# Kernel tuning notes

Measured on AMD Instinct MI355X. Metric: run time of the kernel, lower is better.

The kernel has to match this reference:

```python
import jax, jax.numpy as jnp
import numpy as np

H, D, RPE_DIM, LAYERS = 8, 64, 64, 3
B, N = 8, 4096
EPS = 1e-8


def _srms(x):
    # SimpleRMSNorm: x / (||x||_2 / sqrt(d) + eps) == x / (rms(x) + eps)
    rms = jnp.sqrt(jnp.mean(x * x, axis=-1, keepdims=True))
    return x / (rms + EPS)


def _rpe(pos, w_in, b_in, w_layers, b_layers, w_out, b_out):
    # pos: [nf, 1] -> [nf, H*2*D]
    x = pos @ w_in + b_in
    for i in range(LAYERS):  # fixed small layer count
        x = jax.nn.relu(_srms(x)) @ w_layers[i] + b_layers[i]
    return jax.nn.relu(_srms(x)) @ w_out + b_out


def setup_inputs() -> dict:
    key = jax.random.key(0)
    ks = jax.random.split(key, 4)
    s = 0.02
    return {
        "x": jax.random.normal(ks[0], (B, H, N, D), jnp.float32),
        "w_in": jax.random.normal(ks[1], (1, RPE_DIM), jnp.float32) * s,
        "b_in": jnp.zeros((RPE_DIM,), jnp.float32),
        "w_layers": jax.random.normal(ks[2], (LAYERS, RPE_DIM, RPE_DIM), jnp.float32) * s,
        "b_layers": jnp.zeros((LAYERS, RPE_DIM), jnp.float32),
        "w_out": jax.random.normal(ks[3], (RPE_DIM, H * 2 * D), jnp.float32) * s,
        "b_out": jnp.zeros((H * 2 * D,), jnp.float32),
    }


def reference(x, w_in, b_in, w_layers, b_layers, w_out, b_out):
    # x: [b, h, n, d]; non-causal TnoFD with act_type='none' (identity act_fun)
    n = x.shape[-2]
    fft_size = 2 * n
    nf = fft_size // 2 + 1  # n + 1 frequencies
    pos = jnp.linspace(0.0, np.pi, nf, dtype=x.dtype).reshape(nf, 1)
    res = _rpe(pos, w_in, b_in, w_layers, b_layers, w_out, b_out)  # [nf, H*2D]
    # rearrange 'n (h d) -> h n d'
    res = res.reshape(nf, H, 2 * D).transpose(1, 0, 2)  # [H, nf, 2D]
    real, imag = res[..., :D], res[..., D:]
    imag = imag.at[:, 0, :].set(0.0).at[:, -1, :].set(0.0)
    a = real + 1j * imag  # [H, nf, D] complex filter
    y = jnp.fft.rfft(x, n=fft_size, axis=-2)  # [b, H, nf, D]
    out = jnp.fft.irfft(a * y, n=fft_size, axis=-2)[:, :, :n, :]
    return out.astype(x.dtype)
```

## Files before the change

kernel.cpp:

```cpp
#include <hip/hip_runtime.h>
#include <math.h>


#define PI_F 3.14159265358979323846f
#define TWO_PI_F 6.283185307179586f

__device__ __forceinline__ int r8(int k) {
    return ((k & 7) << 3) | (k >> 3);
}

__global__ __launch_bounds__(512) void gen_tw_kernel(float2* __restrict__ tw4096,
                                                     float2* __restrict__ tw8192,
                                                     float2* __restrict__ e64)
{
    int idx = blockIdx.x * 512 + threadIdx.x;
    if (idx < 4096) {
        float s, c; __sincosf(TWO_PI_F * (float)idx * (1.0f / 4096.0f), &s, &c);
        tw4096[idx] = make_float2(c, s);
    } else if (idx < 8192) {
        int j = idx - 4096;
        float s, c; __sincosf(TWO_PI_F * (float)j * (1.0f / 8192.0f), &s, &c);
        tw8192[j] = make_float2(c, s);
    } else if (idx < 8256) {
        int j = idx - 8192;
        float s, c; __sincosf(TWO_PI_F * (float)j * (1.0f / 64.0f), &s, &c);
        e64[j] = make_float2(c, s);
    }
}

__device__ __forceinline__ void fft8_regs(float2* v, float sgn) {
    float t0r = v[0].x + v[4].x, t0i = v[0].y + v[4].y;
    float t1r = v[0].x - v[4].x, t1i = v[0].y - v[4].y;
    float t2r = v[2].x + v[6].x, t2i = v[2].y + v[6].y;
    float t3r = v[2].x - v[6].x, t3i = v[2].y - v[6].y;
    float e0r = t0r + t2r, e0i = t0i + t2i;
    float e2r = t0r - t2r, e2i = t0i - t2i;
    float e1r = t1r - sgn * t3i, e1i = t1i + sgn * t3r;
    float e3r = t1r + sgn * t3i, e3i = t1i - sgn * t3r;
    float u0r = v[1].x + v[5].x, u0i = v[1].y + v[5].y;
    float u1r = v[1].x - v[5].x, u1i = v[1].y - v[5].y;
    float u2r = v[3].x + v[7].x, u2i = v[3].y + v[7].y;
    float u3r = v[3].x - v[7].x, u3i = v[3].y - v[7].y;
    float o0r = u0r + u2r, o0i = u0i + u2i;
    float o2r = u0r - u2r, o2i = u0i - u2i;
    float o1r = u1r - sgn * u3i, o1i = u1i + sgn * u3r;
    float o3r = u1r + sgn * u3i, o3i = u1i - sgn * u3r;
    const float C = 0.70710678118654752f;
    float w1r = C * (o1r - sgn * o1i), w1i = C * (o1i + sgn * o1r);
    float w2r = -sgn * o2i,            w2i = sgn * o2r;
    float w3r = -C * (o3r + sgn * o3i), w3i = C * (sgn * o3r - o3i);
    v[0] = make_float2(e0r + o0r, e0i + o0i);
    v[4] = make_float2(e0r - o0r, e0i - o0i);
    v[1] = make_float2(e1r + w1r, e1i + w1i);
    v[5] = make_float2(e1r - w1r, e1i - w1i);
    v[2] = make_float2(e2r + w2r, e2i + w2i);
    v[6] = make_float2(e2r - w2r, e2i - w2i);
    v[3] = make_float2(e3r + w3r, e3i + w3i);
    v[7] = make_float2(e3r - w3r, e3i - w3i);
}

__device__ __forceinline__ void fft64_dif(float2* zz, int col, int j0, float sgn,
                                          bool act, const float2* e64s) {
    if (act) {
        #pragma unroll
        for (int jj = 0; jj < 2; ++jj) {
            const int j = j0 + jj * 4;
            float2 v[8];
            #pragma unroll
            for (int r = 0; r < 8; ++r) v[r] = zz[(8 * r + j) * 64 + col];
            fft8_regs(v, sgn);
            #pragma unroll
            for (int r = 1; r < 8; ++r) {
                float2 t = e64s[j * r];
                float c = t.x, s = sgn * t.y;
                float vr = v[r].x, vi = v[r].y;
                v[r] = make_float2(vr * c - vi * s, vr * s + vi * c);
            }
            #pragma unroll
            for (int r = 0; r < 8; ++r) zz[(8 * r + j) * 64 + col] = v[r];
        }
    }
    __syncthreads();
    if (act) {
        #pragma unroll
        for (int jj = 0; jj < 2; ++jj) {
            const int j = j0 + jj * 4;
            float2 v[8];
            #pragma unroll
            for (int r = 0; r < 8; ++r) v[r] = zz[(8 * j + r) * 64 + col];
            fft8_regs(v, sgn);
            #pragma unroll
            for (int r = 0; r < 8; ++r) zz[(8 * j + r) * 64 + col] = v[r];
        }
    }
    __syncthreads();
}

__device__ __forceinline__ void fft64_dit(float2* zz, int col, int j0, float sgn,
                                          bool act, const float2* e64s) {
    if (act) {
        #pragma unroll
        for (int jj = 0; jj < 2; ++jj) {
            const int j = j0 + jj * 4;
            float2 v[8];
            #pragma unroll
            for (int r = 0; r < 8; ++r) v[r] = zz[(8 * j + r) * 64 + col];
            fft8_regs(v, sgn);
            #pragma unroll
            for (int r = 1; r < 8; ++r) {
                float2 t = e64s[j * r];
                float c = t.x, s = sgn * t.y;
                float vr = v[r].x, vi = v[r].y;
                v[r] = make_float2(vr * c - vi * s, vr * s + vi * c);
            }
            #pragma unroll
            for (int r = 0; r < 8; ++r) zz[(8 * j + r) * 64 + col] = v[r];
        }
    }
    __syncthreads();
    if (act) {
        #pragma unroll
        for (int jj = 0; jj < 2; ++jj) {
            const int j = j0 + jj * 4;
            float2 v[8];
            #pragma unroll
            for (int r = 0; r < 8; ++r) v[r] = zz[(8 * r + j) * 64 + col];
            fft8_regs(v, sgn);
            #pragma unroll
            for (int r = 0; r < 8; ++r) zz[(8 * r + j) * 64 + col] = v[r];
        }
    }
    __syncthreads();
}

__global__ __launch_bounds__(256) void mlp_hidden_kernel(
    const float* __restrict__ w_in, const float* __restrict__ b_in,
    const float* __restrict__ w_layers, const float* __restrict__ b_layers,
    float* __restrict__ rbuf)
{
    const int lane = threadIdx.x & 63;
    const int k = blockIdx.x * 4 + (threadIdx.x >> 6);
    if (k > 4096) return;
    const float pos = PI_F * (float)k * (1.0f / 4096.0f);
    float xv = fmaf(pos, w_in[lane], b_in[lane]);
    for (int l = 0; l < 3; ++l) {
        float ss = xv * xv;
        #pragma unroll
        for (int o = 1; o < 64; o <<= 1) ss += __shfl_xor(ss, o, 64);
        float r = xv / (sqrtf(ss * (1.0f / 64.0f)) + 1e-8f);
        r = fmaxf(r, 0.0f);
        const float* W = w_layers + l * 4096;
        float a0 = 0.f, a1 = 0.f, a2 = 0.f, a3 = 0.f;
        for (int i = 0; i < 64; i += 4) {
            a0 = fmaf(__shfl(r, i, 64),     W[(i) * 64 + lane],     a0);
            a1 = fmaf(__shfl(r, i + 1, 64), W[(i + 1) * 64 + lane], a1);
            a2 = fmaf(__shfl(r, i + 2, 64), W[(i + 2) * 64 + lane], a2);
            a3 = fmaf(__shfl(r, i + 3, 64), W[(i + 3) * 64 + lane], a3);
        }
        xv = ((a0 + a1) + (a2 + a3)) + b_layers[l * 64 + lane];
    }
    float ss = xv * xv;
    #pragma unroll
    for (int o = 1; o < 64; o <<= 1) ss += __shfl_xor(ss, o, 64);
    float r = xv / (sqrtf(ss * (1.0f / 64.0f)) + 1e-8f);
    r = fmaxf(r, 0.0f);
    rbuf[(size_t)k * 64 + lane] = r;
}

__global__ __launch_bounds__(256) void mlp_out_kernel(
    const float* __restrict__ rbuf, const float* __restrict__ w_out,
    const float* __restrict__ b_out, float* __restrict__ res)
{
    __shared__ float rl[16 * 64];
    const int tid = threadIdx.x;
    const int nt = blockIdx.x, kt = blockIdx.y;
    for (int it = 0; it < 4; ++it) {
        int idx = it * 256 + tid;
        int row = idx >> 6, i = idx & 63;
        int k = kt * 16 + row;
        rl[idx] = (k <= 4096) ? rbuf[(size_t)k * 64 + i] : 0.0f;
    }
    __syncthreads();
    const int n = nt * 256 + tid;
    float acc[16];
    #pragma unroll
    for (int j = 0; j < 16; ++j) acc[j] = 0.0f;
    for (int i = 0; i < 64; ++i) {
        float wv = w_out[(size_t)i * 1024 + n];
        #pragma unroll
        for (int j = 0; j < 16; ++j)
            acc[j] = fmaf(rl[j * 64 + i], wv, acc[j]);
    }
    float bv = b_out[n];
    for (int j = 0; j < 16; ++j) {
        int k = kt * 16 + j;
        if (k <= 4096) res[(size_t)k * 1024 + n] = acc[j] + bv;
    }
}

__global__ __launch_bounds__(256) void fwd1_kernel(const float* __restrict__ x,
                                                   float2* __restrict__ Y,
                                                   const float2* __restrict__ tw4096,
                                                   const float2* __restrict__ e64g,
                                                   int slab_base)
{
    __shared__ float2 zz[4096];
    __shared__ float2 e64s[64];
    __shared__ float2 twA[64];
    const int tid = threadIdx.x;
    const int m0 = blockIdx.x, lslab = blockIdx.y;
    if (tid < 64) e64s[tid] = e64g[tid];
    else if (tid < 128) twA[tid - 64] = tw4096[m0 * (tid - 64)];
    const float* xs = x + (size_t)(slab_base + lslab) * 262144;
    for (int it = 0; it < 16; ++it) {
        int slot = it * 256 + tid;
        int m1 = slot >> 6, d = slot & 63;
        if (m1 < 32) {
            float vr = xs[(size_t)(128 * m1 + 2 * m0) * 64 + d];
            float vi = xs[(size_t)(128 * m1 + 2 * m0 + 1) * 64 + d];
            zz[slot] = make_float2(vr, vi);
        } else {
            zz[slot] = make_float2(0.0f, 0.0f);
        }
    }
    __syncthreads();
    const int col = tid & 63, j0 = tid >> 6;
    fft64_dif(zz, col, j0, -1.0f, true, e64s);
    float2* Ys = Y + (size_t)lslab * 262144 + (size_t)m0 * 64;
    for (int og = 0; og < 16; ++og) {
        int k1 = og * 4 + j0;
        float2 v = zz[r8(k1) * 64 + col];
        float2 t = twA[k1];
        float c = t.x, s = -t.y;
        Ys[(size_t)k1 * 4096 + col] = make_float2(v.x * c - v.y * s,
                                                  v.x * s + v.y * c);
    }
}

__global__ __launch_bounds__(256) void midspec_kernel(float2* __restrict__ Y,
                                                      const float* __restrict__ res,
                                                      const float2* __restrict__ tw4096,
                                                      const float2* __restrict__ tw8192,
                                                      const float2* __restrict__ e64g,
                                                      int slab_base)
{
    __shared__ float2 zz[4096];
    __shared__ float2 e64s[64];
    __shared__ float2 twS[64];
    __shared__ float2 twB[128];
    const int tid = threadIdx.x;
    const int bx = blockIdx.x;
    const int k1p = bx >> 1, dh = bx & 1;
    const int lslab = blockIdx.y;
    const int h = (slab_base + lslab) & 7;
    const bool pairwg = (k1p >= 1 && k1p <= 31);
    const int k1a = k1p;
    const int k1b = pairwg ? (64 - k1p) : k1p;
    const int NC = pairwg ? 64 : 32;

    if (tid < 64) e64s[tid] = e64g[tid];
    else if (tid < 128) twS[tid - 64] = tw8192[(tid - 64) * 64 + k1a];
    else {
        int i = tid - 128;
        int kk1 = (i < 64) ? k1a : k1b;
        twB[i] = tw4096[(i & 63) * kk1];
    }

    const float4* Pa4 = (const float4*)(Y + (size_t)lslab * 262144 + (size_t)k1a * 4096);
    for (int it = 0; it < 4; ++it) {
        int idx4 = it * 256 + tid;
        int m0 = idx4 >> 4, f = idx4 & 15;
        float4 v = Pa4[m0 * 32 + 16 * dh + f];
        *(float4*)&zz[m0 * 64 + 2 * f] = v;
    }
    if (pairwg) {
        const float4* Pb4 = (const float4*)(Y + (size_t)lslab * 262144 + (size_t)k1b * 4096);
        for (int it = 0; it < 4; ++it) {
            int idx4 = it * 256 + tid;
            int m0 = idx4 >> 4, f = idx4 & 15;
            float4 v = Pb4[m0 * 32 + 16 * dh + f];
            *(float4*)&zz[m0 * 64 + 32 + 2 * f] = v;
        }
    }
    __syncthreads();
    const int col = tid & 63, j0 = tid >> 6;
    fft64_dif(zz, col, j0, -1.0f, col < NC, e64s);

    const int nit = pairwg ? 8 : 4;
    for (int it = 0; it < nit; ++it) {
        int item = it * 256 + tid;
        int k0 = item >> 5, dl = item & 31;
        int c = h * 128 + 32 * dh + dl;
        if (k1p == 0 && k0 == 0) {
            float2 C0 = zz[dl];
            float X0 = C0.x + C0.y, XN = C0.x - C0.y;
            float a0 = res[c], aN = res[(size_t)4096 * 1024 + c];
            float S0 = a0 * X0, SN = aN * XN;
            zz[dl] = make_float2(0.5f * (S0 + SN), 0.5f * (S0 - SN));
            int p2 = 4 * 64 + dl;
            float2 Cq = zz[p2];
            float ar = res[(size_t)2048 * 1024 + c], ai = res[(size_t)2048 * 1024 + c + 64];
            float Sr = ar * Cq.x + ai * Cq.y;
            float Si = ai * Cq.x - ar * Cq.y;
            zz[p2] = make_float2(Sr, -Si);
        } else {
            int k0p, coff;
            if (pairwg)          { k0p = 63 - k0;        coff = 32; }
            else if (k1p == 0)   { k0p = (64 - k0) & 63; coff = 0;  }
            else  { k0p = 63 - k0;        coff = 0;  }
            int sa = r8(k0)  * 64 + dl;
            int sb = r8(k0p) * 64 + coff + dl;
            int k  = k0 * 64 + k1a;
            int km = 4096 - k;
            float2 Ck = zz[sa], Cm = zz[sb];
            float Er = 0.5f * (Ck.x + Cm.x), Ei = 0.5f * (Ck.y - Cm.y);
            float Dr = 0.5f * (Ck.x - Cm.x), Di = 0.5f * (Ck.y + Cm.y);
            float Or = Di, Oi = -Dr;
            float2 tk = twS[k0];
            float cw = tk.x, sw = -tk.y;
            float Tr = Or * cw - Oi * sw, Ti = Or * sw + Oi * cw;
            float Xkr = Er + Tr, Xki = Ei + Ti;
            float Xmr = Er - Tr, Xmi = Ti - Ei;
            float akr = res[(size_t)k * 1024 + c],  aki = res[(size_t)k * 1024 + c + 64];
            float amr = res[(size_t)km * 1024 + c], ami = res[(size_t)km * 1024 + c + 64];
            float Skr = akr * Xkr - aki * Xki, Ski = akr * Xki + aki * Xkr;
            float Smr = amr * Xmr - ami * Xmi, Smi = amr * Xmi + ami * Xmr;
            float Epr = 0.5f * (Skr + Smr), Epi = 0.5f * (Ski - Smi);
            float Ddr = 0.5f * (Skr - Smr), Ddi = 0.5f * (Ski + Smi);
            float Opr = Ddr * cw + Ddi * sw, Opi = Ddi * cw - Ddr * sw;
            zz[sa] = make_float2(Epr - Opi, Epi + Opr);
            zz[sb] = make_float2(Epr + Opi, Opr - Epi);
        }
    }
    __syncthreads();
    fft64_dit(zz, col, j0, +1.0f, col < NC, e64s);

    const int nit2 = pairwg ? 16 : 8;
    for (int it = 0; it < nit2; ++it) {
        int item = it * 256 + tid;
        int pl = item >> 11, rem = item & 2047;
        int m0 = rem >> 5, dl = rem & 31;
        int k1 = pl ? k1b : k1a;
        float2 v = zz[m0 * 64 + pl * 32 + dl];
        float2 t = twB[pl * 64 + m0];
        float c2 = t.x, s = t.y;
        Y[(size_t)lslab * 262144 + (size_t)k1 * 4096 + (size_t)m0 * 64 + 32 * dh + dl] =
            make_float2(v.x * c2 - v.y * s, v.x * s + v.y * c2);
    }
}

__global__ __launch_bounds__(256) void inv2_kernel(const float2* __restrict__ Y,
                                                   float* __restrict__ out,
                                                   const float2* __restrict__ e64g,
                                                   int slab_base)
{
    __shared__ float2 zz[4096];
    __shared__ float2 e64s[64];
    const int tid = threadIdx.x;
    const int m0 = blockIdx.x, lslab = blockIdx.y;
    if (tid < 64) e64s[tid] = e64g[tid];
    const float2* Ys = Y + (size_t)lslab * 262144 + (size_t)m0 * 64;
    const float4* Ys4 = (const float4*)Ys;
    for (int it = 0; it < 8; ++it) {
        int idx4 = it * 256 + tid;
        int k1 = idx4 >> 5, f = idx4 & 31;
        float4 v = Ys4[k1 * 2048 + f];
        *(float4*)&zz[k1 * 64 + 2 * f] = v;
    }
    __syncthreads();
    const int col = tid & 63, j0 = tid >> 6;
    fft64_dif(zz, col, j0, +1.0f, true, e64s);
    float* os = out + (size_t)(slab_base + lslab) * 262144;
    const float sc = 1.0f / 4096.0f;
    for (int it = 0; it < 8; ++it) {
        int slot = it * 256 + tid;
        int m1 = slot >> 6, d = slot & 63;
        float2 v = zz[r8(m1) * 64 + d];
        os[(size_t)(128 * m1 + 2 * m0) * 64 + d]     = v.x * sc;
        os[(size_t)(128 * m1 + 2 * m0 + 1) * 64 + d] = v.y * sc;
    }
}

#define PADF(i) ((i) + ((i) >> 5))

__device__ __forceinline__ unsigned dr4_12(unsigned k) {
    unsigned rb = __brev(k) >> 20;
    return ((rb & 0x555u) << 1) | ((rb >> 1) & 0x555u);
}

__global__ __launch_bounds__(64) void rpe_mlp_kernel(
    const float* __restrict__ w_in, const float* __restrict__ b_in,
    const float* __restrict__ w_layers, const float* __restrict__ b_layers,
    const float* __restrict__ w_out, const float* __restrict__ b_out,
    float* __restrict__ res)
{
    const int k = blockIdx.x;
    const int lane = threadIdx.x;
    const float pos = PI_F * (float)k * (1.0f / 4096.0f);
    float xv = fmaf(pos, w_in[lane], b_in[lane]);
    for (int l = 0; l < 3; ++l) {
        float ss = xv * xv;
        #pragma unroll
        for (int o = 1; o < 64; o <<= 1) ss += __shfl_xor(ss, o, 64);
        float rms = sqrtf(ss * (1.0f / 64.0f));
        float r = xv / (rms + 1e-8f);
        r = r > 0.0f ? r : 0.0f;
        const float* W = w_layers + l * 64 * 64;
        float acc = b_layers[l * 64 + lane];
        for (int i = 0; i < 64; ++i)
            acc = fmaf(__shfl(r, i, 64), W[i * 64 + lane], acc);
        xv = acc;
    }
    float ss = xv * xv;
    #pragma unroll
    for (int o = 1; o < 64; o <<= 1) ss += __shfl_xor(ss, o, 64);
    float rms = sqrtf(ss * (1.0f / 64.0f));
    float r = xv / (rms + 1e-8f);
    r = r > 0.0f ? r : 0.0f;
    float acc[16];
    #pragma unroll
    for (int u = 0; u < 16; ++u) acc[u] = b_out[u * 64 + lane];
    for (int i = 0; i < 64; ++i) {
        float rv = __shfl(r, i, 64);
        const float* Wrow = w_out + i * 1024;
        #pragma unroll
        for (int u = 0; u < 16; ++u)
            acc[u] = fmaf(rv, Wrow[u * 64 + lane], acc[u]);
    }
    float* dst = res + (size_t)k * 1024;
    #pragma unroll
    for (int u = 0; u < 16; ++u) dst[u * 64 + lane] = acc[u];
}

__global__ __launch_bounds__(256) void fftconv_kernel(
    const float* __restrict__ x, const float* __restrict__ res,
    float* __restrict__ out)
{
    __shared__ float re[PADF(4095) + 1];
    __shared__ float im[PADF(4095) + 1];
    const int tid = threadIdx.x;
    const int blk = blockIdx.x;
    const int d = (blk >> 3) & 63;
    const int slab = (blk & 7) | ((blk >> 9) << 3);
    const int h = slab & 7;
    const size_t base = (size_t)slab * 4096 * 64 + (size_t)d;
    const float* xc = x + base;
    float* oc = out + base;
    const int c = h * 128 + d;
    for (int m = tid; m < 2048; m += 256) {
        re[PADF(m)] = xc[(size_t)(2 * m) * 64];
        im[PADF(m)] = xc[(size_t)(2 * m + 1) * 64];
    }
    for (int m = 2048 + tid; m < 4096; m += 256) { re[PADF(m)] = 0.0f; im[PADF(m)] = 0.0f; }
    __syncthreads();
    for (int S = 1024; S >= 1; S >>= 2) {
        const float ab = -TWO_PI_F / (float)(4 * S);
        for (int j = tid; j < 1024; j += 256) {
            const int q = j & (S - 1);
            const int i0 = ((j & ~(S - 1)) << 2) | q;
            const int p0 = PADF(i0), p1 = PADF(i0 + S), p2 = PADF(i0 + 2 * S), p3 = PADF(i0 + 3 * S);
            float x0r = re[p0], x0i = im[p0], x1r = re[p1], x1i = im[p1];
            float x2r = re[p2], x2i = im[p2], x3r = re[p3], x3i = im[p3];
            float A0r = x0r + x2r, A0i = x0i + x2i, A1r = x0r - x2r, A1i = x0i - x2i;
            float A2r = x1r + x3r, A2i = x1i + x3i, A3r = x1r - x3r, A3i = x1i - x3i;
            float s1, c1; __sincosf(ab * (float)q, &s1, &c1);
            float c2 = c1 * c1 - s1 * s1, s2 = 2.0f * c1 * s1;
            float c3 = c2 * c1 - s2 * s1, s3 = s2 * c1 + c2 * s1;
            re[p0] = A0r + A2r; im[p0] = A0i + A2i;
            float t1r = A1r + A3i, t1i = A1i - A3r;
            re[p1] = t1r * c1 - t1i * s1; im[p1] = t1r * s1 + t1i * c1;
            float t2r = A0r - A2r, t2i = A0i - A2i;
            re[p2] = t2r * c2 - t2i * s2; im[p2] = t2r * s2 + t2i * c2;
            float t3r = A1r - A3i, t3i = A1i + A3r;
            re[p3] = t3r * c3 - t3i * s3; im[p3] = t3r * s3 + t3i * c3;
        }
        __syncthreads();
    }
    for (int k = tid; k <= 2048; k += 256) {
        if (k == 0) {
            float C0r = re[0], C0i = im[0];
            float X0 = C0r + C0i, XN = C0r - C0i;
            float a0 = res[c], aN = res[(size_t)4096 * 1024 + c];
            float S0 = a0 * X0, SN = aN * XN;
            re[0] = 0.5f * (S0 + SN); im[0] = 0.5f * (S0 - SN);
        } else if (k == 2048) {
            const int p = PADF(2);
            float Cr = re[p], Ci = im[p];
            float ar = res[(size_t)2048 * 1024 + c], ai = res[(size_t)2048 * 1024 + c + 64];
            float Sr = ar * Cr + ai * Ci, Si = ai * Cr - ar * Ci;
            re[p] = Sr; im[p] = -Si;
        } else {
            const int pk = PADF((int)dr4_12((unsigned)k));
            const int pm = PADF((int)dr4_12((unsigned)(4096 - k)));
            float Ckr = re[pk], Cki = im[pk];
            float Cmr = re[pm], Cmi = im[pm];
            float Er = 0.5f * (Ckr + Cmr), Ei = 0.5f * (Cki - Cmi);
            float Dr = 0.5f * (Ckr - Cmr), Di = 0.5f * (Cki + Cmi);
            float Or = Di, Oi = -Dr;
            float sw, cw; __sincosf(-TWO_PI_F * (float)k * (1.0f / 8192.0f), &sw, &cw);
            float Tr = Or * cw - Oi * sw, Ti = Or * sw + Oi * cw;
            float Xkr = Er + Tr, Xki = Ei + Ti;
            float Xmr = Er - Tr, Xmi = Ti - Ei;
            float akr = res[(size_t)k * 1024 + c], aki = res[(size_t)k * 1024 + c + 64];
            float amr = res[(size_t)(4096 - k) * 1024 + c], ami = res[(size_t)(4096 - k) * 1024 + c + 64];
            float Skr = akr * Xkr - aki * Xki, Ski = akr * Xki + aki * Xkr;
            float Smr = amr * Xmr - ami * Xmi, Smi = amr * Xmi + ami * Xmr;
            float Epr = 0.5f * (Skr + Smr), Epi = 0.5f * (Ski - Smi);
            float Ddr = 0.5f * (Skr - Smr), Ddi = 0.5f * (Ski + Smi);
            float Opr = Ddr * cw + Ddi * sw, Opi = Ddi * cw - Ddr * sw;
            re[pk] = Epr - Opi; im[pk] = Epi + Opr;
            re[pm] = Epr + Opi; im[pm] = Opr - Epi;
        }
    }
    __syncthreads();
    for (int S = 1; S <= 1024; S <<= 2) {
        const float ab = TWO_PI_F / (float)(4 * S);
        for (int j = tid; j < 1024; j += 256) {
            const int q = j & (S - 1);
            const int i0 = ((j & ~(S - 1)) << 2) | q;
            const int p0 = PADF(i0), p1 = PADF(i0 + S), p2 = PADF(i0 + 2 * S), p3 = PADF(i0 + 3 * S);
            float y0r = re[p0], y0i = im[p0], y1r = re[p1], y1i = im[p1];
            float y2r = re[p2], y2i = im[p2], y3r = re[p3], y3i = im[p3];
            float s1, c1; __sincosf(ab * (float)q, &s1, &c1);
            float c2 = c1 * c1 - s1 * s1, s2 = 2.0f * c1 * s1;
            float c3 = c2 * c1 - s2 * s1, s3 = s2 * c1 + c2 * s1;
            float x1r = y1r * c1 - y1i * s1, x1i = y1r * s1 + y1i * c1;
            float x2r = y2r * c2 - y2i * s2, x2i = y2r * s2 + y2i * c2;
            float x3r = y3r * c3 - y3i * s3, x3i = y3r * s3 + y3i * c3;
            float B0r = y0r + x2r, B0i = y0i + x2i, B1r = y0r - x2r, B1i = y0i - x2i;
            float B2r = x1r + x3r, B2i = x1i + x3i, B3r = x1r - x3r, B3i = x1i - x3i;
            re[p0] = B0r + B2r; im[p0] = B0i + B2i;
            re[p1] = B1r - B3i; im[p1] = B1i + B3r;
            re[p2] = B0r - B2r; im[p2] = B0i - B2i;
            re[p3] = B1r + B3i; im[p3] = B1i - B3r;
        }
        __syncthreads();
    }
    const float sc = 1.0f / 4096.0f;
    for (int m = tid; m < 2048; m += 256) {
        oc[(size_t)(2 * m) * 64]     = re[PADF(m)] * sc;
        oc[(size_t)(2 * m + 1) * 64] = im[PADF(m)] * sc;
    }
}

extern "C" void kernel_launch(void* const* d_in, const int* in_sizes, int n_in,
                              void* d_out, int out_size, void* d_ws, size_t ws_size,
                              hipStream_t stream) {
    const float* x        = (const float*)d_in[0];
    const float* w_in     = (const float*)d_in[1];
    const float* b_in     = (const float*)d_in[2];
    const float* w_layers = (const float*)d_in[3];
    const float* b_layers = (const float*)d_in[4];
    const float* w_out    = (const float*)d_in[5];
    const float* b_out    = (const float*)d_in[6];
    float* out = (float*)d_out;
    float* wsf = (float*)d_ws;

    const size_t off_res    = 0;
    const size_t off_r      = 4195328;
    const size_t off_tw4096 = 4457536;
    const size_t off_tw8192 = off_tw4096 + 8192;
    const size_t off_e64    = off_tw8192 + 8192;
    const size_t off_Y      = off_e64 + 192;
    const size_t Y_PER_SLAB = 524288;

    float* res = wsf + off_res;
    const size_t avail_f = ws_size / 4;
    int nc = 0;
    if (avail_f > off_Y)
        nc = (int)((avail_f - off_Y) / Y_PER_SLAB);
    if (nc > 64) nc = 64;

    if (nc >= 1) {
        float2* tw4096 = (float2*)(wsf + off_tw4096);
        float2* tw8192 = (float2*)(wsf + off_tw8192);
        float2* e64    = (float2*)(wsf + off_e64);
        float2* Y      = (float2*)(wsf + off_Y);
        gen_tw_kernel<<<17, 512, 0, stream>>>(tw4096, tw8192, e64);
        mlp_hidden_kernel<<<1025, 256, 0, stream>>>(w_in, b_in, w_layers, b_layers,
                                                    wsf + off_r);
        mlp_out_kernel<<<dim3(4, 257), 256, 0, stream>>>(wsf + off_r, w_out, b_out, res);
        for (int s0 = 0; s0 < 64; s0 += nc) {
            int cur = (64 - s0 < nc) ? (64 - s0) : nc;
            fwd1_kernel<<<dim3(64, cur), 256, 0, stream>>>(x, Y, tw4096, e64, s0);
            midspec_kernel<<<dim3(66, cur), 256, 0, stream>>>(Y, res, tw4096, tw8192,
                                                              e64, s0);
            inv2_kernel<<<dim3(64, cur), 256, 0, stream>>>(Y, out, e64, s0);
        }
    } else {
        rpe_mlp_kernel<<<4097, 64, 0, stream>>>(w_in, b_in, w_layers, b_layers,
                                                w_out, b_out, res);
        fftconv_kernel<<<4096, 256, 0, stream>>>(x, res, out);
    }
}
```

Baseline: 274.2 us.

## Halve per-block column width in FFT kernels to cut LDS and raise occupancy

The three FFT-convolution kernels now give each block half as many feature columns (32 instead of 64, or 16 pair-columns in midspec). Each thread handles one radix-8 group instead of two, and the grids double. This halves shared memory per block and sets a launch-bounds minimum of 8 blocks per CU, so more waves can be resident to hide memory latency. The forward kernel also skips loading the zero-padded upper half by zero-filling those inputs in registers. The cost is more blocks and repeated twiddle and setup work per block.

```diff
diff --git a/kernel.cpp b/kernel.cpp
--- a/kernel.cpp
+++ b/kernel.cpp
@@ -59,76 +59,64 @@
     v[7] = make_float2(e3r - w3r, e3i - w3i);
 }
 
-__device__ __forceinline__ void fft64_dif(float2* zz, int col, int j0, float sgn,
-                                          bool act, const float2* e64s) {
+template<bool ZUP>
+__device__ __forceinline__ void fft64_dif32(float2* zz, int col, int j, float sgn,
+                                            bool act, const float2* e64s) {
     if (act) {
-        #pragma unroll
-        for (int jj = 0; jj < 2; ++jj) {
-            const int j = j0 + jj * 4;
-            float2 v[8];
-            #pragma unroll
-            for (int r = 0; r < 8; ++r) v[r] = zz[(8 * r + j) * 64 + col];
-            fft8_regs(v, sgn);
-            #pragma unroll
-            for (int r = 1; r < 8; ++r) {
-                float2 t = e64s[j * r];
-                float c = t.x, s = sgn * t.y;
-                float vr = v[r].x, vi = v[r].y;
-                v[r] = make_float2(vr * c - vi * s, vr * s + vi * c);
-            }
-            #pragma unroll
-            for (int r = 0; r < 8; ++r) zz[(8 * r + j) * 64 + col] = v[r];
-        }
+        float2 v[8];
+        #pragma unroll
+        for (int r = 0; r < 8; ++r) {
+            if (ZUP && r >= 4) v[r] = make_float2(0.0f, 0.0f);
+            else v[r] = zz[(8 * r + j) * 32 + col];
+        }
+        fft8_regs(v, sgn);
+        #pragma unroll
+        for (int r = 1; r < 8; ++r) {
+            float2 t = e64s[j * r];
+            float c = t.x, s = sgn * t.y;
+            float vr = v[r].x, vi = v[r].y;
+            v[r] = make_float2(vr * c - vi * s, vr * s + vi * c);
+        }
+        #pragma unroll
+        for (int r = 0; r < 8; ++r) zz[(8 * r + j) * 32 + col] = v[r];
     }
     __syncthreads();
     if (act) {
-        #pragma unroll
-        for (int jj = 0; jj < 2; ++jj) {
-            const int j = j0 + jj * 4;
-            float2 v[8];
-            #pragma unroll
-            for (int r = 0; r < 8; ++r) v[r] = zz[(8 * j + r) * 64 + col];
-            fft8_regs(v, sgn);
-            #pragma unroll
-            for (int r = 0; r < 8; ++r) zz[(8 * j + r) * 64 + col] = v[r];
-        }
-    }
-    __syncthreads();
-}
-
-__device__ __forceinline__ void fft64_dit(float2* zz, int col, int j0, float sgn,
-                                          bool act, const float2* e64s) {
+        float2 v[8];
+        #pragma unroll
+        for (int r = 0; r < 8; ++r) v[r] = zz[(8 * j + r) * 32 + col];
+        fft8_regs(v, sgn);
+        #pragma unroll
+        for (int r = 0; r < 8; ++r) zz[(8 * j + r) * 32 + col] = v[r];
+    }
+    __syncthreads();
+}
+
+__device__ __forceinline__ void fft64_dit32(float2* zz, int col, int j, float sgn,
+                                            bool act, const float2* e64s) {
     if (act) {
-        #pragma unroll
-        for (int jj = 0; jj < 2; ++jj) {
-            const int j = j0 + jj * 4;
-            float2 v[8];
-            #pragma unroll
-            for (int r = 0; r < 8; ++r) v[r] = zz[(8 * j + r) * 64 + col];
-            fft8_regs(v, sgn);
-            #pragma unroll
-            for (int r = 1; r < 8; ++r) {
-                float2 t = e64s[j * r];
-                float c = t.x, s = sgn * t.y;
-                float vr = v[r].x, vi = v[r].y;
-                v[r] = make_float2(vr * c - vi * s, vr * s + vi * c);
-            }
-            #pragma unroll
-            for (int r = 0; r < 8; ++r) zz[(8 * j + r) * 64 + col] = v[r];
-        }
+        float2 v[8];
+        #pragma unroll
+        for (int r = 0; r < 8; ++r) v[r] = zz[(8 * j + r) * 32 + col];
+        fft8_regs(v, sgn);
+        #pragma unroll
+        for (int r = 1; r < 8; ++r) {
+            float2 t = e64s[j * r];
+            float c = t.x, s = sgn * t.y;
+            float vr = v[r].x, vi = v[r].y;
+            v[r] = make_float2(vr * c - vi * s, vr * s + vi * c);
+        }
+        #pragma unroll
+        for (int r = 0; r < 8; ++r) zz[(8 * j + r) * 32 + col] = v[r];
     }
     __syncthreads();
     if (act) {
-        #pragma unroll
-        for (int jj = 0; jj < 2; ++jj) {
-            const int j = j0 + jj * 4;
-            float2 v[8];
-            #pragma unroll
-            for (int r = 0; r < 8; ++r) v[r] = zz[(8 * r + j) * 64 + col];
-            fft8_regs(v, sgn);
-            #pragma unroll
-            for (int r = 0; r < 8; ++r) zz[(8 * r + j) * 64 + col] = v[r];
-        }
+        float2 v[8];
+        #pragma unroll
+        for (int r = 0; r < 8; ++r) v[r] = zz[(8 * r + j) * 32 + col];
+        fft8_regs(v, sgn);
+        #pragma unroll
+        for (int r = 0; r < 8; ++r) zz[(8 * r + j) * 32 + col] = v[r];
     }
     __syncthreads();
 }
@@ -198,38 +186,36 @@
     }
 }
 
-__global__ __launch_bounds__(256) void fwd1_kernel(const float* __restrict__ x,
-                                                   float2* __restrict__ Y,
-                                                   const float2* __restrict__ tw4096,
-                                                   const float2* __restrict__ e64g,
-                                                   int slab_base)
-{
-    __shared__ float2 zz[4096];
+__global__ __launch_bounds__(256, 8) void fwd1_kernel(const float* __restrict__ x,
+                                                      float2* __restrict__ Y,
+                                                      const float2* __restrict__ tw4096,
+                                                      const float2* __restrict__ e64g,
+                                                      int slab_base)
+{
+    __shared__ float2 zz[64 * 32];
     __shared__ float2 e64s[64];
     __shared__ float2 twA[64];
     const int tid = threadIdx.x;
-    const int m0 = blockIdx.x, lslab = blockIdx.y;
+    const int bx = blockIdx.x;
+    const int m0 = bx >> 1, dh = bx & 1;
+    const int lslab = blockIdx.y;
     if (tid < 64) e64s[tid] = e64g[tid];
     else if (tid < 128) twA[tid - 64] = tw4096[m0 * (tid - 64)];
-    const float* xs = x + (size_t)(slab_base + lslab) * 262144;
-    for (int it = 0; it < 16; ++it) {
+    const float* xs = x + (size_t)(slab_base + lslab) * 262144 + 32 * dh;
+    for (int it = 0; it < 4; ++it) {
         int slot = it * 256 + tid;
-        int m1 = slot >> 6, d = slot & 63;
-        if (m1 < 32) {
-            float vr = xs[(size_t)(128 * m1 + 2 * m0) * 64 + d];
-            float vi = xs[(size_t)(128 * m1 + 2 * m0 + 1) * 64 + d];
-            zz[slot] = make_float2(vr, vi);
-        } else {
-            zz[slot] = make_float2(0.0f, 0.0f);
-        }
-    }
-    __syncthreads();
-    const int col = tid & 63, j0 = tid >> 6;
-    fft64_dif(zz, col, j0, -1.0f, true, e64s);
-    float2* Ys = Y + (size_t)lslab * 262144 + (size_t)m0 * 64;
-    for (int og = 0; og < 16; ++og) {
-        int k1 = og * 4 + j0;
-        float2 v = zz[r8(k1) * 64 + col];
+        int m1 = slot >> 5, dd = slot & 31;
+        float vr = xs[(size_t)(128 * m1 + 2 * m0) * 64 + dd];
+        float vi = xs[(size_t)(128 * m1 + 2 * m0 + 1) * 64 + dd];
+        zz[slot] = make_float2(vr, vi);
+    }
+    __syncthreads();
+    const int col = tid & 31, j = tid >> 5;
+    fft64_dif32<true>(zz, col, j, -1.0f, true, e64s);
+    float2* Ys = Y + (size_t)lslab * 262144 + (size_t)m0 * 64 + 32 * dh;
+    for (int og = 0; og < 8; ++og) {
+        int k1 = og * 8 + j;
+        float2 v = zz[r8(k1) * 32 + col];
         float2 t = twA[k1];
         float c = t.x, s = -t.y;
         Ys[(size_t)k1 * 4096 + col] = make_float2(v.x * c - v.y * s,
@@ -237,26 +223,26 @@
     }
 }
 
-__global__ __launch_bounds__(256) void midspec_kernel(float2* __restrict__ Y,
-                                                      const float* __restrict__ res,
-                                                      const float2* __restrict__ tw4096,
-                                                      const float2* __restrict__ tw8192,
-                                                      const float2* __restrict__ e64g,
-                                                      int slab_base)
-{
-    __shared__ float2 zz[4096];
+__global__ __launch_bounds__(256, 8) void midspec_kernel(float2* __restrict__ Y,
+                                                         const float* __restrict__ res,
+                                                         const float2* __restrict__ tw4096,
+                                                         const float2* __restrict__ tw8192,
+                                                         const float2* __restrict__ e64g,
+                                                         int slab_base)
+{
+    __shared__ float2 zz[64 * 32];
     __shared__ float2 e64s[64];
     __shared__ float2 twS[64];
     __shared__ float2 twB[128];
     const int tid = threadIdx.x;
     const int bx = blockIdx.x;
-    const int k1p = bx >> 1, dh = bx & 1;
+    const int k1p = bx >> 2, dq = bx & 3;
     const int lslab = blockIdx.y;
     const int h = (slab_base + lslab) & 7;
     const bool pairwg = (k1p >= 1 && k1p <= 31);
     const int k1a = k1p;
     const int k1b = pairwg ? (64 - k1p) : k1p;
-    const int NC = pairwg ? 64 : 32;
+    const int NC = pairwg ? 32 : 16;
 
     if (tid < 64) e64s[tid] = e64g[tid];
     else if (tid < 128) twS[tid - 64] = tw8192[(tid - 64) * 64 + k1a];
@@ -267,37 +253,37 @@
     }
 
     const float4* Pa4 = (const float4*)(Y + (size_t)lslab * 262144 + (size_t)k1a * 4096);
-    for (int it = 0; it < 4; ++it) {
+    for (int it = 0; it < 2; ++it) {
         int idx4 = it * 256 + tid;
-        int m0 = idx4 >> 4, f = idx4 & 15;
-        float4 v = Pa4[m0 * 32 + 16 * dh + f];
-        *(float4*)&zz[m0 * 64 + 2 * f] = v;
+        int m0 = idx4 >> 3, f = idx4 & 7;
+        float4 v = Pa4[m0 * 32 + 8 * dq + f];
+        *(float4*)&zz[m0 * 32 + 2 * f] = v;
     }
     if (pairwg) {
         const float4* Pb4 = (const float4*)(Y + (size_t)lslab * 262144 + (size_t)k1b * 4096);
-        for (int it = 0; it < 4; ++it) {
+        for (int it = 0; it < 2; ++it) {
             int idx4 = it * 256 + tid;
-            int m0 = idx4 >> 4, f = idx4 & 15;
-            float4 v = Pb4[m0 * 32 + 16 * dh + f];
-            *(float4*)&zz[m0 * 64 + 32 + 2 * f] = v;
-        }
-    }
-    __syncthreads();
-    const int col = tid & 63, j0 = tid >> 6;
-    fft64_dif(zz, col, j0, -1.0f, col < NC, e64s);
-
-    const int nit = pairwg ? 8 : 4;
+            int m0 = idx4 >> 3, f = idx4 & 7;
+            float4 v = Pb4[m0 * 32 + 8 * dq + f];
+            *(float4*)&zz[m0 * 32 + 16 + 2 * f] = v;
+        }
+    }
+    __syncthreads();
+    const int col = tid & 31, j = tid >> 5;
+    fft64_dif32<false>(zz, col, j, -1.0f, col < NC, e64s);
+
+    const int nit = pairwg ? 4 : 2;
     for (int it = 0; it < nit; ++it) {
         int item = it * 256 + tid;
-        int k0 = item >> 5, dl = item & 31;
-        int c = h * 128 + 32 * dh + dl;
+        int k0 = item >> 4, dl = item & 15;
+        int c = h * 128 + 16 * dq + dl;
         if (k1p == 0 && k0 == 0) {
             float2 C0 = zz[dl];
             float X0 = C0.x + C0.y, XN = C0.x - C0.y;
             float a0 = res[c], aN = res[(size_t)4096 * 1024 + c];
             float S0 = a0 * X0, SN = aN * XN;
             zz[dl] = make_float2(0.5f * (S0 + SN), 0.5f * (S0 - SN));
-            int p2 = 4 * 64 + dl;
+            int p2 = 4 * 32 + dl;
             float2 Cq = zz[p2];
             float ar = res[(size_t)2048 * 1024 + c], ai = res[(size_t)2048 * 1024 + c + 64];
             float Sr = ar * Cq.x + ai * Cq.y;
@@ -305,11 +291,11 @@
             zz[p2] = make_float2(Sr, -Si);
         } else {
             int k0p, coff;
-            if (pairwg)          { k0p = 63 - k0;        coff = 32; }
+            if (pairwg)          { k0p = 63 - k0;        coff = 16; }
             else if (k1p == 0)   { k0p = (64 - k0) & 63; coff = 0;  }
             else  { k0p = 63 - k0;        coff = 0;  }
-            int sa = r8(k0)  * 64 + dl;
-            int sb = r8(k0p) * 64 + coff + dl;
+            int sa = r8(k0)  * 32 + dl;
+            int sb = r8(k0p) * 32 + coff + dl;
             int k  = k0 * 64 + k1a;
             int km = 4096 - k;
             float2 Ck = zz[sa], Cm = zz[sb];
@@ -333,51 +319,52 @@
         }
     }
     __syncthreads();
-    fft64_dit(zz, col, j0, +1.0f, col < NC, e64s);
-
-    const int nit2 = pairwg ? 16 : 8;
+    fft64_dit32(zz, col, j, +1.0f, col < NC, e64s);
+
+    const int nit2 = pairwg ? 8 : 4;
     for (int it = 0; it < nit2; ++it) {
         int item = it * 256 + tid;
-        int pl = item >> 11, rem = item & 2047;
-        int m0 = rem >> 5, dl = rem & 31;
+        int pl = item >> 10, rem = item & 1023;
+        int m0 = rem >> 4, dl = rem & 15;
         int k1 = pl ? k1b : k1a;
-        float2 v = zz[m0 * 64 + pl * 32 + dl];
+        float2 v = zz[m0 * 32 + pl * 16 + dl];
         float2 t = twB[pl * 64 + m0];
         float c2 = t.x, s = t.y;
-        Y[(size_t)lslab * 262144 + (size_t)k1 * 4096 + (size_t)m0 * 64 + 32 * dh + dl] =
+        Y[(size_t)lslab * 262144 + (size_t)k1 * 4096 + (size_t)m0 * 64 + 16 * dq + dl] =
             make_float2(v.x * c2 - v.y * s, v.x * s + v.y * c2);
     }
 }
 
-__global__ __launch_bounds__(256) void inv2_kernel(const float2* __restrict__ Y,
-                                                   float* __restrict__ out,
-                                                   const float2* __restrict__ e64g,
-                                                   int slab_base)
-{
-    __shared__ float2 zz[4096];
+__global__ __launch_bounds__(256, 8) void inv2_kernel(const float2* __restrict__ Y,
+                                                      float* __restrict__ out,
+                                                      const float2* __restrict__ e64g,
+                                                      int slab_base)
+{
+    __shared__ float2 zz[64 * 32];
     __shared__ float2 e64s[64];
     const int tid = threadIdx.x;
-    const int m0 = blockIdx.x, lslab = blockIdx.y;
+    const int bx = blockIdx.x;
+    const int m0 = bx >> 1, dh = bx & 1;
+    const int lslab = blockIdx.y;
     if (tid < 64) e64s[tid] = e64g[tid];
-    const float2* Ys = Y + (size_t)lslab * 262144 + (size_t)m0 * 64;
-    const float4* Ys4 = (const float4*)Ys;
-    for (int it = 0; it < 8; ++it) {
+    const float4* Ys4 = (const float4*)(Y + (size_t)lslab * 262144 + (size_t)m0 * 64);
+    for (int it = 0; it < 4; ++it) {
         int idx4 = it * 256 + tid;
-        int k1 = idx4 >> 5, f = idx4 & 31;
-        float4 v = Ys4[k1 * 2048 + f];
-        *(float4*)&zz[k1 * 64 + 2 * f] = v;
-    }
-    __syncthreads();
-    const int col = tid & 63, j0 = tid >> 6;
-    fft64_dif(zz, col, j0, +1.0f, true, e64s);
-    float* os = out + (size_t)(slab_base + lslab) * 262144;
+        int k1 = idx4 >> 4, f = idx4 & 15;
+        float4 v = Ys4[k1 * 2048 + 16 * dh + f];
+        *(float4*)&zz[k1 * 32 + 2 * f] = v;
+    }
+    __syncthreads();
+    const int col = tid & 31, j = tid >> 5;
+    fft64_dif32<false>(zz, col, j, +1.0f, true, e64s);
+    float* os = out + (size_t)(slab_base + lslab) * 262144 + 32 * dh;
     const float sc = 1.0f / 4096.0f;
-    for (int it = 0; it < 8; ++it) {
+    for (int it = 0; it < 4; ++it) {
         int slot = it * 256 + tid;
-        int m1 = slot >> 6, d = slot & 63;
-        float2 v = zz[r8(m1) * 64 + d];
-        os[(size_t)(128 * m1 + 2 * m0) * 64 + d]     = v.x * sc;
-        os[(size_t)(128 * m1 + 2 * m0 + 1) * 64 + d] = v.y * sc;
+        int m1 = slot >> 5, dd = slot & 31;
+        float2 v = zz[r8(m1) * 32 + dd];
+        os[(size_t)(128 * m1 + 2 * m0) * 64 + dd]     = v.x * sc;
+        os[(size_t)(128 * m1 + 2 * m0 + 1) * 64 + dd] = v.y * sc;
     }
 }
 
@@ -582,10 +569,10 @@
         mlp_out_kernel<<<dim3(4, 257), 256, 0, stream>>>(wsf + off_r, w_out, b_out, res);
         for (int s0 = 0; s0 < 64; s0 += nc) {
             int cur = (64 - s0 < nc) ? (64 - s0) : nc;
-            fwd1_kernel<<<dim3(64, cur), 256, 0, stream>>>(x, Y, tw4096, e64, s0);
-            midspec_kernel<<<dim3(66, cur), 256, 0, stream>>>(Y, res, tw4096, tw8192,
-                                                              e64, s0);
-            inv2_kernel<<<dim3(64, cur), 256, 0, stream>>>(Y, out, e64, s0);
+            fwd1_kernel<<<dim3(128, cur), 256, 0, stream>>>(x, Y, tw4096, e64, s0);
+            midspec_kernel<<<dim3(132, cur), 256, 0, stream>>>(Y, res, tw4096, tw8192,
+                                                               e64, s0);
+            inv2_kernel<<<dim3(128, cur), 256, 0, stream>>>(Y, out, e64, s0);
         }
     } else {
         rpe_mlp_kernel<<<4097, 64, 0, stream>>>(w_in, b_in, w_layers, b_layers,
```

Result: slower. 281.8 us (+2.8%).
